# Kernel optimization log

Hardware: AMD Instinct MI355X
Metric: run time of the kernel (lower is better)

## Reference

```python
import jax, jax.numpy as jnp
import numpy as np
import math


def setup_inputs() -> dict:
    key = jax.random.key(0)
    kq, kk, kv = jax.random.split(key, 3)
    B, HQ, HKV, S, D = 1, 32, 8, 2048, 128
    query = jax.random.normal(kq, (B, HQ, S, D), dtype=jnp.float32)
    key_s = jax.random.normal(kk, (B, HKV, S, D), dtype=jnp.float32)
    value = jax.random.normal(kv, (B, HKV, S, D), dtype=jnp.float32)
    # additive causal mask [B,1,S,S]: 0 where j<=i, large-negative elsewhere
    neg = jnp.finfo(jnp.float32).min
    i = jnp.arange(S)
    attention_mask = jnp.where(i[None, :] <= i[:, None], 0.0, neg).astype(jnp.float32)[None, None]
    return {"query": query, "key": key_s, "value": value,
            "attention_mask": attention_mask, "window_size": 1024}


def reference(query, key, value, attention_mask, window_size):
    B, HQ, S, D = query.shape
    groups = HQ // key.shape[1]
    scaling = 1.0 / math.sqrt(D)
    # repeat_kv (GQA -> MHA)
    k = jnp.repeat(key, groups, axis=1)   # [B,HQ,S,D]
    v = jnp.repeat(value, groups, axis=1)
    # ---- eager_attention_forward ----
    scores = jnp.einsum('bhqd,bhkd->bhqk', query, k) * scaling
    scores = scores + attention_mask[:, :, :, :S]
    attn_weights = jax.nn.softmax(scores.astype(jnp.float32), axis=-1).astype(query.dtype)
    attn_output = jnp.einsum('bhqk,bhkd->bhqd', attn_weights, v)
    attn_output = attn_output.transpose(0, 2, 1, 3)  # [B,S,HQ,D]
    # ---- compute_window_attn_weights ----
    W = window_size
    qw = query[:, :, -W:, :]                                  # [B,HQ,W,D]
    ww = jnp.einsum('bhqd,bhkd->bhqk', qw, k) / math.sqrt(D)  # [B,HQ,W,S]
    neg = jnp.finfo(ww.dtype).min
    r = jnp.arange(W)
    win_mask = jnp.where(r[None, :] <= r[:, None], 0.0, neg).astype(ww.dtype)  # [W,W]
    ww = ww.at[:, :, :, -W:].add(win_mask[None, None])
    window_attn_weights = jax.nn.softmax(ww.astype(jnp.float32), axis=-1).astype(query.dtype)
    return (attn_output, attn_weights, window_attn_weights)
```

## Files before the change

kernel.cpp:

```cpp
#include <hip/hip_runtime.h>
#include <hip/hip_bf16.h>

typedef __bf16 bf16x8 __attribute__((ext_vector_type(8)));
typedef float f32x4 __attribute__((ext_vector_type(4)));
static_assert(sizeof(bf16x8) == 16, "bf16x8 must be 16B");

constexpr int S = 2048, D = 128, HQ = 32, W = 1024;
constexpr float SCALE_L2E = 0.08838834764831845f * 1.4426950408889634f;

constexpr size_t O1 = (size_t)S * HQ * D;
constexpr size_t O2 = O1 + (size_t)HQ * S * S;
constexpr int TILE64 = 64 * 256;
constexpr int TILE32 = 32 * 256;

__device__ __forceinline__ void gl_lds16(const void* g, void* l) {
    __builtin_amdgcn_global_load_lds(
        (const __attribute__((address_space(1))) void*)(unsigned long long)g,
        (__attribute__((address_space(3))) void*)(unsigned int)(unsigned long long)l,
        16, 0, 0);
}
__device__ __forceinline__ void st4(float* p, f32x4 v) {
    *reinterpret_cast<f32x4*>(p) = v;
}

__global__ __launch_bounds__(256)
void prep_kernel(const float* __restrict__ K, const float* __restrict__ V,
                 char* __restrict__ KbI, char* __restrict__ VtI)
{
    __shared__ __attribute__((aligned(16))) __bf16 Vs[128][72];
    const int b = blockIdx.x, hkv = b >> 5, kt = b & 31;
    const int tid = threadIdx.x;
    const float* Ks   = K + ((size_t)hkv * S + kt * 64) * D;
    const float* Vsrc = V + ((size_t)hkv * S + kt * 64) * D;
    char* Kimg = KbI + (size_t)(hkv * 32 + kt) * TILE64;
    char* Vimg = VtI + (size_t)(hkv * 32 + kt) * TILE64;

    #pragma unroll
    for (int i = 0; i < 4; ++i) {
        int idx = tid + i * 256;
        int r = idx >> 4, sl = idx & 15;
        float4 a = *reinterpret_cast<const float4*>(Ks + r * D + sl * 8);
        float4 c = *reinterpret_cast<const float4*>(Ks + r * D + sl * 8 + 4);
        bf16x8 f = {(__bf16)a.x, (__bf16)a.y, (__bf16)a.z, (__bf16)a.w,
                    (__bf16)c.x, (__bf16)c.y, (__bf16)c.z, (__bf16)c.w};
        *reinterpret_cast<bf16x8*>(Kimg + r * 256 + ((sl * 16) ^ ((r & 7) << 4))) = f;
    }
    #pragma unroll
    for (int i = 0; i < 8; ++i) {
        int idx = tid + i * 256;
        int r = idx >> 5, c = (idx & 31) * 4;
        float4 vv = *reinterpret_cast<const float4*>(Vsrc + r * D + c);
        Vs[c + 0][r] = (__bf16)vv.x; Vs[c + 1][r] = (__bf16)vv.y;
        Vs[c + 2][r] = (__bf16)vv.z; Vs[c + 3][r] = (__bf16)vv.w;
    }
    __syncthreads();
    #pragma unroll
    for (int i = 0; i < 4; ++i) {
        int idx = tid + i * 256;
        int img = idx >> 9;
        int rem = idx & 511;
        int d = rem >> 2, sl = rem & 3;
        bf16x8 v = *reinterpret_cast<const bf16x8*>(&Vs[d][img * 32 + sl * 8]);
        *reinterpret_cast<bf16x8*>(Vimg + img * TILE32 + d * 64 + ((sl * 16) ^ ((d & 3) << 4))) = v;
    }
}

__global__ __launch_bounds__(256, 4)
void attn_fused5(const float* __restrict__ Q, const char* __restrict__ KbI,
                 const char* __restrict__ VtI, float* __restrict__ out)
{
    __shared__ __attribute__((aligned(16))) char BUF[4][TILE32];
    __shared__ __attribute__((aligned(16))) char PST[4][1024];

    const int bid = blockIdx.x;
    const int j   = bid >> 5;
    const int qt = (j < 8) ? (16 + j) : (j < 16) ? (23 - j) : (j < 24) ? (47 - j) : (j - 24);
    const int b5 = bid & 31;
    const int h  = (b5 & 7) * 4 + (b5 >> 3);
    const int hkv = h >> 2;
    const int q0  = qt << 6;
    const int tid = threadIdx.x, wave = tid >> 6, lane = tid & 63;
    const int lo = lane & 15, hi = lane >> 4;
    const int qw0 = q0 + wave * 16;
    const bool winw = (qt >= 16);

    const char* Ktiles = KbI + (size_t)hkv * 32 * TILE64;
    const char* Vtiles = VtI + (size_t)hkv * 32 * TILE64;
    const float* Qh = Q + (size_t)h * S * D;

    bf16x8 qf[4];
    {
        const float* qs = Qh + (size_t)(qw0 + lo) * D + hi * 8;
        #pragma unroll
        for (int dc = 0; dc < 4; ++dc) {
            float4 a = *reinterpret_cast<const float4*>(qs + dc * 32);
            float4 b = *reinterpret_cast<const float4*>(qs + dc * 32 + 4);
            bf16x8 f;
            f[0] = (__bf16)(a.x * SCALE_L2E); f[1] = (__bf16)(a.y * SCALE_L2E);
            f[2] = (__bf16)(a.z * SCALE_L2E); f[3] = (__bf16)(a.w * SCALE_L2E);
            f[4] = (__bf16)(b.x * SCALE_L2E); f[5] = (__bf16)(b.y * SCALE_L2E);
            f[6] = (__bf16)(b.z * SCALE_L2E); f[7] = (__bf16)(b.w * SCALE_L2E);
            qf[dc] = f;
        }
    }

    float lsum[4] = {0.f, 0.f, 0.f, 0.f};
    {
        #pragma unroll
        for (int i = 0; i < 4; ++i)
            gl_lds16(Ktiles + (wave * 4 + i) * 1024 + lane * 16,
                     &BUF[0][0] + (wave * 4 + i) * 1024);
        __builtin_amdgcn_sched_barrier(0);
        asm volatile("s_waitcnt vmcnt(0)" ::: "memory");
        __builtin_amdgcn_s_barrier();
        __builtin_amdgcn_sched_barrier(0);

        int cur = 0;
        for (int kt = 0; kt <= qt; ++kt) {
            if (kt < qt) {
                const char* src = Ktiles + (size_t)(kt + 1) * TILE64;
                char* dst = &BUF[(cur ^ 1) * 2][0];
                #pragma unroll
                for (int i = 0; i < 4; ++i)
                    gl_lds16(src + (wave * 4 + i) * 1024 + lane * 16, dst + (wave * 4 + i) * 1024);
                __builtin_amdgcn_sched_barrier(0);
            }
            const char* KtB = &BUF[cur * 2][0];
            #pragma unroll
            for (int cg = 0; cg < 4; ++cg) {
                f32x4 acc = {0.f, 0.f, 0.f, 0.f};
                const int row = cg * 16 + lo, swzr = (row & 7) << 4;
                #pragma unroll
                for (int dc = 0; dc < 4; ++dc) {
                    bf16x8 kf = *reinterpret_cast<const bf16x8*>(
                        KtB + row * 256 + ((hi * 16 + dc * 64) ^ swzr));
                    acc = __builtin_amdgcn_mfma_f32_16x16x32_bf16(qf[dc], kf, acc, 0, 0, 0);
                }
                const int k = (kt << 6) + cg * 16 + lo;
                #pragma unroll
                for (int r = 0; r < 4; ++r) {
                    int q = qw0 + hi * 4 + r;
                    lsum[r] += (k <= q) ? exp2f(acc[r]) : 0.f;
                }
            }
            __builtin_amdgcn_sched_barrier(0);
            asm volatile("s_waitcnt vmcnt(0) lgkmcnt(0)" ::: "memory");
            __builtin_amdgcn_s_barrier();
            __builtin_amdgcn_sched_barrier(0);
            cur ^= 1;
        }
    }
    float rcp_[4];
    #pragma unroll
    for (int r = 0; r < 4; ++r) {
        float v = lsum[r];
        v += __shfl_xor(v, 1); v += __shfl_xor(v, 2);
        v += __shfl_xor(v, 4); v += __shfl_xor(v, 8);
        rcp_[r] = 1.0f / v;
    }

    f32x4 oacc[8];
    #pragma unroll
    for (int i = 0; i < 8; ++i) oacc[i] = (f32x4){0.f, 0.f, 0.f, 0.f};
    char* Ps = PST[wave];
    const int nk32 = (qt + 1) * 2;

    {
        #pragma unroll
        for (int i = 0; i < 2; ++i) {
            gl_lds16(Ktiles + (wave * 2 + i) * 1024 + lane * 16, &BUF[0][0] + (wave * 2 + i) * 1024);
            gl_lds16(Vtiles + (wave * 2 + i) * 1024 + lane * 16, &BUF[2][0] + (wave * 2 + i) * 1024);
        }
        __builtin_amdgcn_sched_barrier(0);
        asm volatile("s_waitcnt vmcnt(0)" ::: "memory");
        __builtin_amdgcn_s_barrier();
        __builtin_amdgcn_sched_barrier(0);
    }

    int cur = 0;
    for (int t = 0; t < nk32; ++t) {
        const bool more = (t + 1 < nk32);
        if (more) {
            const char* sk = Ktiles + (size_t)(t + 1) * TILE32;
            const char* sv = Vtiles + (size_t)(t + 1) * TILE32;
            char* dk = &BUF[cur ^ 1][0];
            char* dv = &BUF[2 + (cur ^ 1)][0];
            #pragma unroll
            for (int i = 0; i < 2; ++i) {
                gl_lds16(sk + (wave * 2 + i) * 1024 + lane * 16, dk + (wave * 2 + i) * 1024);
                gl_lds16(sv + (wave * 2 + i) * 1024 + lane * 16, dv + (wave * 2 + i) * 1024);
            }
            __builtin_amdgcn_sched_barrier(0);
        }
        const char* KtB = &BUF[cur][0];
        const char* VtB = &BUF[2 + cur][0];
        const int kbase = t * 32;

        #pragma unroll
        for (int cg = 0; cg < 2; ++cg) {
            f32x4 acc = {0.f, 0.f, 0.f, 0.f};
            const int row = cg * 16 + lo, swzr = (row & 7) << 4;
            #pragma unroll
            for (int dc = 0; dc < 4; ++dc) {
                bf16x8 kf = *reinterpret_cast<const bf16x8*>(
                    KtB + row * 256 + ((hi * 16 + dc * 64) ^ swzr));
                acc = __builtin_amdgcn_mfma_f32_16x16x32_bf16(qf[dc], kf, acc, 0, 0, 0);
            }
            const int k = kbase + cg * 16 + lo;
            #pragma unroll
            for (int r = 0; r < 4; ++r) {
                const int q = qw0 + hi * 4 + r;
                float pv = (k <= q) ? exp2f(acc[r]) * rcp_[r] : 0.f;
                const int prow = hi * 4 + r;
                *reinterpret_cast<__bf16*>(
                    Ps + prow * 64 + ((2 * (cg * 16 + lo)) ^ ((prow & 3) << 4))) = (__bf16)pv;
            }
        }

        {
            const int row = lane >> 2;
            const int sl  = lane & 3;
            const int q = qw0 + row;
            bf16x8 pv8 = *reinterpret_cast<const bf16x8*>(
                Ps + row * 64 + ((sl * 16) ^ ((row & 3) << 4)));
            f32x4 f0 = {(float)pv8[0], (float)pv8[1], (float)pv8[2], (float)pv8[3]};
            f32x4 f1 = {(float)pv8[4], (float)pv8[5], (float)pv8[6], (float)pv8[7]};
            float* dstP = out + O1 + ((size_t)h * S + q) * S + kbase + sl * 8;
            st4(dstP, f0);
            st4(dstP + 4, f1);
            if (winw) {
                float* dstW = out + O2 + ((size_t)h * W + (q - W)) * S + kbase + sl * 8;
                st4(dstW, f0);
                st4(dstW + 4, f1);
            }
        }

        {
            bf16x8 pf = *reinterpret_cast<const bf16x8*>(
                Ps + lo * 64 + ((hi * 16) ^ ((lo & 3) << 4)));
            #pragma unroll
            for (int dg = 0; dg < 8; ++dg) {
                const int d = dg * 16 + lo;
                bf16x8 vf = *reinterpret_cast<const bf16x8*>(
                    VtB + d * 64 + ((hi * 16) ^ ((d & 3) << 4)));
                oacc[dg] = __builtin_amdgcn_mfma_f32_16x16x32_bf16(pf, vf, oacc[dg], 0, 0, 0);
            }
        }

        if (more) {
            __builtin_amdgcn_sched_barrier(0);
            if (winw) asm volatile("s_waitcnt vmcnt(4) lgkmcnt(0)" ::: "memory");
            else      asm volatile("s_waitcnt vmcnt(2) lgkmcnt(0)" ::: "memory");
            __builtin_amdgcn_s_barrier();
            __builtin_amdgcn_sched_barrier(0);
        }
        cur ^= 1;
    }

    {
        const int zr = lane >> 2;
        const int c0 = (lane & 3) * 16;
        const f32x4 z = {0.f, 0.f, 0.f, 0.f};
        const int q = qw0 + zr;
        for (int kt = qt + 1; kt < 32; ++kt) {
            float* dp = out + O1 + ((size_t)h * S + q) * S + kt * 64 + c0;
            #pragma unroll
            for (int jj = 0; jj < 4; ++jj) st4(dp + jj * 4, z);
            if (winw) {
                float* dw = out + O2 + ((size_t)h * W + (q - W)) * S + kt * 64 + c0;
                #pragma unroll
                for (int jj = 0; jj < 4; ++jj) st4(dw + jj * 4, z);
            }
        }
    }

    #pragma unroll
    for (int dg = 0; dg < 8; ++dg) {
        #pragma unroll
        for (int r = 0; r < 4; ++r) {
            const int q = qw0 + hi * 4 + r;
            out[((size_t)q * HQ + h) * D + dg * 16 + lo] = oacc[dg][r];
        }
    }
}

extern "C" void kernel_launch(void* const* d_in, const int* in_sizes, int n_in,
                              void* d_out, int out_size, void* d_ws, size_t ws_size,
                              hipStream_t stream)
{
    const float* Q = (const float*)d_in[0];
    const float* K = (const float*)d_in[1];
    const float* V = (const float*)d_in[2];
    float* out = (float*)d_out;

    char* KbI = (char*)d_ws;
    char* VtI = (char*)d_ws + (size_t)4 * 1024 * 1024;

    hipLaunchKernelGGL(prep_kernel, dim3(256),  dim3(256), 0, stream, K, V, KbI, VtI);
    hipLaunchKernelGGL(attn_fused5, dim3(1024), dim3(256), 0, stream, Q, KbI, VtI, out);
}
```

Baseline: 277.0 us.

## Split fused attention into separate row-sum and main attention kernels

Splits the fused kernel into two launches. The first computes the softmax denominators (exp-sum over keys) and writes reciprocals to a workspace buffer. The second reads them and computes probabilities, outputs and weights. Each kernel gets a simpler register and LDS footprint, and the sum kernel uses larger single K tiles. In exchange it adds a launch, a global round trip for the reciprocals, and a reload of Q in the second kernel.

```diff
diff --git a/kernel.cpp b/kernel.cpp
--- a/kernel.cpp
+++ b/kernel.cpp
@@ -66,11 +66,10 @@
 }
 
 __global__ __launch_bounds__(256, 4)
-void attn_fused5(const float* __restrict__ Q, const char* __restrict__ KbI,
-                 const char* __restrict__ VtI, float* __restrict__ out)
+void lsum_kernel(const float* __restrict__ Q, const char* __restrict__ KbI,
+                 float* __restrict__ lsr)
 {
-    __shared__ __attribute__((aligned(16))) char BUF[4][TILE32];
-    __shared__ __attribute__((aligned(16))) char PST[4][1024];
+    __shared__ __attribute__((aligned(16))) char BUF[2][TILE64];
 
     const int bid = blockIdx.x;
     const int j   = bid >> 5;
@@ -78,14 +77,11 @@
     const int b5 = bid & 31;
     const int h  = (b5 & 7) * 4 + (b5 >> 3);
     const int hkv = h >> 2;
-    const int q0  = qt << 6;
     const int tid = threadIdx.x, wave = tid >> 6, lane = tid & 63;
     const int lo = lane & 15, hi = lane >> 4;
-    const int qw0 = q0 + wave * 16;
-    const bool winw = (qt >= 16);
+    const int qw0 = (qt << 6) + wave * 16;
 
     const char* Ktiles = KbI + (size_t)hkv * 32 * TILE64;
-    const char* Vtiles = VtI + (size_t)hkv * 32 * TILE64;
     const float* Qh = Q + (size_t)h * S * D;
 
     bf16x8 qf[4];
@@ -119,13 +115,13 @@
         for (int kt = 0; kt <= qt; ++kt) {
             if (kt < qt) {
                 const char* src = Ktiles + (size_t)(kt + 1) * TILE64;
-                char* dst = &BUF[(cur ^ 1) * 2][0];
+                char* dst = &BUF[cur ^ 1][0];
                 #pragma unroll
                 for (int i = 0; i < 4; ++i)
                     gl_lds16(src + (wave * 4 + i) * 1024 + lane * 16, dst + (wave * 4 + i) * 1024);
                 __builtin_amdgcn_sched_barrier(0);
             }
-            const char* KtB = &BUF[cur * 2][0];
+            const char* KtB = &BUF[cur][0];
             #pragma unroll
             for (int cg = 0; cg < 4; ++cg) {
                 f32x4 acc = {0.f, 0.f, 0.f, 0.f};
@@ -150,13 +146,58 @@
             cur ^= 1;
         }
     }
-    float rcp_[4];
     #pragma unroll
     for (int r = 0; r < 4; ++r) {
         float v = lsum[r];
         v += __shfl_xor(v, 1); v += __shfl_xor(v, 2);
         v += __shfl_xor(v, 4); v += __shfl_xor(v, 8);
-        rcp_[r] = 1.0f / v;
+        if (lo == 0) lsr[h * S + qw0 + hi * 4 + r] = 1.0f / v;
+    }
+}
+
+__global__ __launch_bounds__(256, 4)
+void attn_main(const float* __restrict__ Q, const char* __restrict__ KbI,
+               const char* __restrict__ VtI, const float* __restrict__ lsr,
+               float* __restrict__ out)
+{
+    __shared__ __attribute__((aligned(16))) char BUF[4][TILE32];
+    __shared__ __attribute__((aligned(16))) char PST[4][1024];
+
+    const int bid = blockIdx.x;
+    const int j   = bid >> 5;
+    const int qt = (j < 8) ? (16 + j) : (j < 16) ? (23 - j) : (j < 24) ? (47 - j) : (j - 24);
+    const int b5 = bid & 31;
+    const int h  = (b5 & 7) * 4 + (b5 >> 3);
+    const int hkv = h >> 2;
+    const int q0  = qt << 6;
+    const int tid = threadIdx.x, wave = tid >> 6, lane = tid & 63;
+    const int lo = lane & 15, hi = lane >> 4;
+    const int qw0 = q0 + wave * 16;
+    const bool winw = (qt >= 16);
+
+    const char* Ktiles = KbI + (size_t)hkv * 32 * TILE64;
+    const char* Vtiles = VtI + (size_t)hkv * 32 * TILE64;
+    const float* Qh = Q + (size_t)h * S * D;
+
+    bf16x8 qf[4];
+    {
+        const float* qs = Qh + (size_t)(qw0 + lo) * D + hi * 8;
+        #pragma unroll
+        for (int dc = 0; dc < 4; ++dc) {
+            float4 a = *reinterpret_cast<const float4*>(qs + dc * 32);
+            float4 b = *reinterpret_cast<const float4*>(qs + dc * 32 + 4);
+            bf16x8 f;
+            f[0] = (__bf16)(a.x * SCALE_L2E); f[1] = (__bf16)(a.y * SCALE_L2E);
+            f[2] = (__bf16)(a.z * SCALE_L2E); f[3] = (__bf16)(a.w * SCALE_L2E);
+            f[4] = (__bf16)(b.x * SCALE_L2E); f[5] = (__bf16)(b.y * SCALE_L2E);
+            f[6] = (__bf16)(b.z * SCALE_L2E); f[7] = (__bf16)(b.w * SCALE_L2E);
+            qf[dc] = f;
+        }
+    }
+    float rcp_[4];
+    {
+        float4 rc = *reinterpret_cast<const float4*>(lsr + h * S + qw0 + hi * 4);
+        rcp_[0] = rc.x; rcp_[1] = rc.y; rcp_[2] = rc.z; rcp_[3] = rc.w;
     }
 
     f32x4 oacc[8];
@@ -293,9 +334,11 @@
     const float* V = (const float*)d_in[2];
     float* out = (float*)d_out;
 
-    char* KbI = (char*)d_ws;
-    char* VtI = (char*)d_ws + (size_t)4 * 1024 * 1024;
+    char*  KbI = (char*)d_ws;
+    char*  VtI = (char*)d_ws + (size_t)4 * 1024 * 1024;
+    float* lsr = (float*)((char*)d_ws + (size_t)8 * 1024 * 1024);
 
     hipLaunchKernelGGL(prep_kernel, dim3(256),  dim3(256), 0, stream, K, V, KbI, VtI);
-    hipLaunchKernelGGL(attn_fused5, dim3(1024), dim3(256), 0, stream, Q, KbI, VtI, out);
-}
+    hipLaunchKernelGGL(lsum_kernel, dim3(1024), dim3(256), 0, stream, Q, KbI, lsr);
+    hipLaunchKernelGGL(attn_main,   dim3(1024), dim3(256), 0, stream, Q, KbI, VtI, lsr, out);
+}
```

New measurement: 306.3 us. 10.6% more time.
